# Performance work log

Hardware: AMD Instinct MI355X
Metric: run time of the kernel (lower is better)

Reference implementation:

```python
import jax, jax.numpy as jnp
import numpy as np

N_NODES = 50000
N_PATHS = 4
N_EDGES = 800000
D_IN = 256
D_OUT = 256
D_HID = 128  # SemanticAttention default hidden_size


def setup_inputs() -> dict:
    key = jax.random.key(0)
    ks = jax.random.split(key, 6)
    x = jax.random.normal(ks[0], (N_NODES, D_IN), dtype=jnp.float32)
    edge_indices = jax.random.randint(ks[1], (N_PATHS, 2, N_EDGES), 0, N_NODES)
    Ws = jax.random.normal(ks[2], (N_PATHS, D_IN, D_OUT), dtype=jnp.float32) * (1.0 / np.sqrt(D_IN))
    bs = jnp.zeros((N_PATHS, D_OUT), dtype=jnp.float32)
    attn_w1 = jax.random.normal(ks[3], (D_OUT, D_HID), dtype=jnp.float32) * (1.0 / np.sqrt(D_OUT))
    attn_b1 = jnp.zeros((D_HID,), dtype=jnp.float32)
    attn_w2 = jax.random.normal(ks[4], (D_HID, 1), dtype=jnp.float32) * (1.0 / np.sqrt(D_HID))
    return {"x": x, "edge_indices": edge_indices, "Ws": Ws, "bs": bs,
            "attn_w1": attn_w1, "attn_b1": attn_b1, "attn_w2": attn_w2}


def _gcn_conv(x, W, b, edges):
    """PyG GCNConv with normalize=True, add_self_loops=True.
    out = D^{-1/2} (A + I) D^{-1/2} (x @ W) + b
    """
    n = x.shape[0]
    xw = x @ W  # [N, D_OUT]
    loop = jnp.arange(n, dtype=edges.dtype)
    src = jnp.concatenate([edges[0], loop])
    dst = jnp.concatenate([edges[1], loop])
    ones = jnp.ones(src.shape[0], dtype=x.dtype)
    deg = jax.ops.segment_sum(ones, dst, num_segments=n)  # in-degree incl. self loop
    dinv = jnp.where(deg > 0, jax.lax.rsqrt(deg), 0.0)
    norm = dinv[src] * dinv[dst]  # [E+N]
    msgs = xw[src] * norm[:, None]  # gather + scale
    return jax.ops.segment_sum(msgs, dst, num_segments=n) + b  # scatter-add


def reference(x, edge_indices, Ws, bs, attn_w1, attn_b1, attn_w2):
    P = edge_indices.shape[0]
    # per-meta-path GCN embeddings, stacked -> [N, P, D_OUT]
    z = jnp.stack([_gcn_conv(x, Ws[i], bs[i], edge_indices[i]) for i in range(P)], axis=1)
    # semantic attention: per-node softmax over meta-paths
    w = jnp.tanh(z @ attn_w1 + attn_b1) @ attn_w2  # [N, P, 1]
    beta = jax.nn.softmax(w, axis=1)
    return (beta * z).sum(axis=1)  # [N, D_OUT]
```

## Files before the change

### kernel.cpp

```cpp
#include <hip/hip_runtime.h>
#include <hip/hip_fp16.h>
#include <cstdint>
#include <cstddef>

#define NN 50000
#define NE 800000
#define NP 4
#define DD 256
#define HH 128
#define MPAD 50048
#define PADIDX 50000

#define NB 196
#define CAP 5120
#define SCAP 6144
#define EPB 4096
#define NBB ((NE + EPB - 1) / EPB)
#define BIN_BLOCKS (NBB * NP)

typedef _Float16 f16x8 __attribute__((ext_vector_type(8)));
typedef float f32x4 __attribute__((ext_vector_type(4)));

#define X_OCT (NN * DD / 8)
#define XP_OCT (MPAD * DD / 8)
#define W_OCT (NP * DD * DD / 8)
#define W1_OCT (HH * DD / 8)
#define CVT_BLOCKS ((XP_OCT + W_OCT + W1_OCT + 255) / 256)
#define GEMM_BLOCKS ((MPAD / 64) * NP)

__global__ __launch_bounds__(256) void k_bin(const int* __restrict__ edges,
                                             int* __restrict__ gcnt,
                                             unsigned int* __restrict__ binned,
                                             const float* __restrict__ x,
                                             const float* __restrict__ Ws,
                                             const float* __restrict__ w1,
                                             _Float16* __restrict__ xh,
                                             _Float16* __restrict__ Wt,
                                             _Float16* __restrict__ w1t) {
    const int bx = blockIdx.x;
    const int tid = threadIdx.x;
    if (bx < BIN_BLOCKS) {
        __shared__ int hist[256], lb[256], cur[256], gbase[256], wsum[4];
        __shared__ unsigned int stage[EPB];
        const int p  = bx / NBB;
        const int bc = bx - p * NBB;
        const int e0 = bc * EPB;
        const int total = min(EPB, NE - e0);
        const int* es = edges + (size_t)p * 2 * NE;
        const int* ed = es + NE;
        hist[tid] = 0;
        __syncthreads();
        unsigned int word[16];
        int bkt[16];
#pragma unroll
        for (int j = 0; j < 16; j++) {
            int e = e0 + j * 256 + tid;
            bkt[j] = -1;
            if (e < NE) {
                int dst = ed[e];
                int src = es[e];
                int b = dst >> 8;
                bkt[j] = b;
                word[j] = ((unsigned)b << 24) | ((unsigned)(dst & 255) << 16) | (unsigned)src;
                atomicAdd(&hist[b], 1);
            }
        }
        __syncthreads();
        const int lane = tid & 63, wv = tid >> 6;
        int v = hist[tid];
        int incl = v;
#pragma unroll
        for (int off = 1; off < 64; off <<= 1) {
            int u = __shfl_up(incl, off);
            if (lane >= off) incl += u;
        }
        if (lane == 63) wsum[wv] = incl;
        __syncthreads();
        int wbase = 0;
        for (int i = 0; i < wv; i++) wbase += wsum[i];
        int excl = wbase + incl - v;
        lb[tid] = excl;
        cur[tid] = excl;
        if (tid < NB && v > 0) gbase[tid] = atomicAdd(&gcnt[p * NB + tid], v);
        __syncthreads();
#pragma unroll
        for (int j = 0; j < 16; j++)
            if (bkt[j] >= 0) {
                int r = atomicAdd(&cur[bkt[j]], 1);
                stage[r] = word[j];
            }
        __syncthreads();
        for (int s = tid; s < total; s += 256) {
            unsigned int wd = stage[s];
            int b = wd >> 24;
            int posl = gbase[b] + (s - lb[b]);
            if (posl < CAP)
                binned[(size_t)(p * NB + b) * CAP + posl] = wd & 0x00FFFFFFu;
        }
        return;
    }
    int i = (bx - BIN_BLOCKS) * 256 + tid;
    if (i < XP_OCT) {
        f16x8 o;
        if (i < X_OCT) {
            const float4* src = (const float4*)x + (size_t)i * 2;
            float4 v0 = src[0], v1 = src[1];
            o[0] = (_Float16)v0.x; o[1] = (_Float16)v0.y; o[2] = (_Float16)v0.z; o[3] = (_Float16)v0.w;
            o[4] = (_Float16)v1.x; o[5] = (_Float16)v1.y; o[6] = (_Float16)v1.z; o[7] = (_Float16)v1.w;
        } else {
#pragma unroll
            for (int t = 0; t < 8; t++) o[t] = (_Float16)0.0f;
        }
        *((f16x8*)xh + i) = o;
    } else if (i < XP_OCT + W_OCT) {
        int j = i - XP_OCT;
        int p   = j / (DD * DD / 8);
        int rem = j - p * (DD * DD / 8);
        int n   = rem >> 5;
        int k8  = (rem & 31) * 8;
        const float* wp = Ws + (size_t)p * DD * DD;
        f16x8 o;
#pragma unroll
        for (int t = 0; t < 8; t++) o[t] = (_Float16)wp[(size_t)(k8 + t) * DD + n];
        *((f16x8*)(Wt + (size_t)p * DD * DD + (size_t)n * DD + k8)) = o;
    } else if (i < XP_OCT + W_OCT + W1_OCT) {
        int j = i - XP_OCT - W_OCT;
        int n  = j >> 5;
        int k8 = (j & 31) * 8;
        f16x8 o;
#pragma unroll
        for (int t = 0; t < 8; t++) o[t] = (_Float16)w1[(size_t)(k8 + t) * HH + n];
        *((f16x8*)(w1t + (size_t)n * DD + k8)) = o;
    }
}

__global__ __launch_bounds__(256) void k_sort(const int* __restrict__ gcnt,
                                              const unsigned int* __restrict__ binned,
                                              unsigned short* __restrict__ srcs,
                                              int* __restrict__ offs,
                                              int* __restrict__ ends,
                                              float* __restrict__ dinv) {
    __shared__ int hist[256], cur[256], wsum[4];
    __shared__ unsigned short sorted[SCAP];
    const int bx = blockIdx.x;
    const int tid = threadIdx.x;
    const int p = bx / NB, b = bx - p * NB;
    const int base = bx * SCAP;
    const int n = min(gcnt[bx], CAP);
    hist[tid] = 0;
#pragma unroll
    for (int j = 0; j < SCAP / 256; j++) sorted[j * 256 + tid] = (unsigned short)PADIDX;
    __syncthreads();
    unsigned int w[20];
#pragma unroll
    for (int j = 0; j < 20; j++) {
        int s = j * 256 + tid;
        w[j] = 0xFFFFFFFFu;
        if (s < n) {
            w[j] = binned[(size_t)bx * CAP + s];
            atomicAdd(&hist[(w[j] >> 16) & 255], 1);
        }
    }
    __syncthreads();
    const int lane = tid & 63, wv = tid >> 6;
    int v  = hist[tid];
    int pv = (v + 7) & ~7;
    int incl = pv;
#pragma unroll
    for (int off = 1; off < 64; off <<= 1) {
        int u = __shfl_up(incl, off);
        if (lane >= off) incl += u;
    }
    if (lane == 63) wsum[wv] = incl;
    __syncthreads();
    int wbase = 0;
    for (int i = 0; i < wv; i++) wbase += wsum[i];
    int excl = wbase + incl - pv;
    cur[tid] = excl;
    const int node = b * 256 + tid;
    if (node < NN) {
        int o = base + excl;
        offs[p * NN + node] = o;
        ends[p * NN + node] = o + pv;
        dinv[p * NN + node] = rsqrtf((float)v + 1.0f);
    }
    __syncthreads();
    int totalpad = wsum[0] + wsum[1] + wsum[2] + wsum[3];
#pragma unroll
    for (int j = 0; j < 20; j++)
        if (w[j] != 0xFFFFFFFFu) {
            int r = atomicAdd(&cur[(w[j] >> 16) & 255], 1);
            if (r < SCAP) sorted[r] = (unsigned short)(w[j] & 0xFFFFu);
        }
    __syncthreads();
#pragma unroll
    for (int j = 0; j < SCAP / 256; j++) {
        int s = j * 256 + tid;
        if (s < totalpad && s < SCAP) srcs[base + s] = sorted[s];
    }
}

__global__ __launch_bounds__(256) void k_gemm(const _Float16* __restrict__ xh,
                                              const _Float16* __restrict__ Wt,
                                              const float* __restrict__ dinv,
                                              _Float16* __restrict__ xws) {
    const int gb   = blockIdx.x;
    const int p    = gb / (MPAD / 64);
    const int bm   = gb - p * (MPAD / 64);
    const int wv   = threadIdx.x >> 6;
    const int lane = threadIdx.x & 63;
    const int m_base = bm * 64;
    const int n0   = wv * 64;
    const int mr   = lane & 15;
    const int quad = lane >> 4;

    const _Float16* ap = xh + (size_t)(m_base + mr) * DD + quad * 8;
    const _Float16* bp = Wt + (size_t)p * DD * DD + (size_t)(n0 + mr) * DD + quad * 8;
    const float* dv = dinv + (size_t)p * NN;
    _Float16* cp = xws + (size_t)p * MPAD * DD;

    f32x4 acc[4][4] = {};
    for (int k0 = 0; k0 < DD; k0 += 32) {
        f16x8 a[4], b[4];
#pragma unroll
        for (int i = 0; i < 4; i++) a[i] = *(const f16x8*)(ap + (size_t)i * 16 * DD + k0);
#pragma unroll
        for (int j = 0; j < 4; j++) b[j] = *(const f16x8*)(bp + (size_t)j * 16 * DD + k0);
#pragma unroll
        for (int i = 0; i < 4; i++)
#pragma unroll
            for (int j = 0; j < 4; j++)
                acc[i][j] = __builtin_amdgcn_mfma_f32_16x16x32_f16(a[i], b[j], acc[i][j], 0, 0, 0);
    }
#pragma unroll
    for (int i = 0; i < 4; i++) {
#pragma unroll
        for (int r = 0; r < 4; r++) {
            int row = m_base + i * 16 + quad * 4 + r;
            float d = (row < NN) ? dv[row] : 0.0f;
#pragma unroll
            for (int j = 0; j < 4; j++)
                cp[(size_t)row * DD + n0 + j * 16 + mr] = (_Float16)(d * acc[i][j][r]);
        }
    }
}

__global__ __launch_bounds__(512) void k_fused(const _Float16* __restrict__ xws,
                                               const float* __restrict__ dinv,
                                               const int* __restrict__ offs,
                                               const int* __restrict__ ends,
                                               const unsigned short* __restrict__ srcs,
                                               const float* __restrict__ bs,
                                               const _Float16* __restrict__ w1t,
                                               const float* __restrict__ b1,
                                               const float* __restrict__ w2,
                                               float* __restrict__ out) {
    const int w    = threadIdx.x >> 6;
    const int lane = threadIdx.x & 63;
    const int quad = lane >> 4, mr = lane & 15;
    const int half = lane >> 5, hl = lane & 31;

    __shared__ __align__(16) _Float16 zs[64][264];

    union U { f16x8 v; int i4[4]; };

#pragma unroll 1
    for (int q = 0; q < 2; q++) {
        const int n = blockIdx.x * 16 + w * 2 + q;
#pragma unroll 1
        for (int p = 0; p < NP; p++) {
            const _Float16* xp = xws + (size_t)p * MPAD * DD;
            U acc;
#pragma unroll
            for (int t = 0; t < 4; t++) acc.i4[t] = 0;
            if (half == 0)
                acc.v = *(const f16x8*)(xp + (size_t)n * DD + hl * 8);
            int k  = offs[p * NN + n];
            int ke = ends[p * NN + n];
            for (; k + 16 <= ke; k += 16) {
                int s[8];
#pragma unroll
                for (int j = 0; j < 8; j++) s[j] = srcs[k + 2 * j + half];
                f16x8 v[8];
#pragma unroll
                for (int j = 0; j < 8; j++)
                    v[j] = *(const f16x8*)(xp + (size_t)s[j] * DD + hl * 8);
                acc.v += ((v[0] + v[1]) + (v[2] + v[3])) + ((v[4] + v[5]) + (v[6] + v[7]));
            }
            if (k < ke) {
                int s[4];
#pragma unroll
                for (int j = 0; j < 4; j++) s[j] = srcs[k + 2 * j + half];
                f16x8 v[4];
#pragma unroll
                for (int j = 0; j < 4; j++)
                    v[j] = *(const f16x8*)(xp + (size_t)s[j] * DD + hl * 8);
                acc.v += (v[0] + v[1]) + (v[2] + v[3]);
            }
            U other;
#pragma unroll
            for (int t = 0; t < 4; t++) other.i4[t] = __shfl_xor(acc.i4[t], 32);
            acc.v += other.v;
            if (half == 0) {
                float dvv = dinv[p * NN + n];
                int row = (w * 2 + q) * 4 + p;
                f16x8 zo;
#pragma unroll
                for (int t = 0; t < 8; t++)
                    zo[t] = (_Float16)(dvv * (float)acc.v[t] + bs[p * DD + hl * 8 + t]);
                *(f16x8*)&zs[row][hl * 8] = zo;
            }
        }
    }

    __syncthreads();
    if (w >= 4) return;

    f32x4 acch[8] = {};
    for (int k0 = 0; k0 < DD; k0 += 32) {
        f16x8 a = *(const f16x8*)&zs[w * 16 + mr][k0 + quad * 8];
#pragma unroll
        for (int j = 0; j < 8; j++) {
            f16x8 b = *(const f16x8*)(w1t + (size_t)(j * 16 + mr) * DD + k0 + quad * 8);
            acch[j] = __builtin_amdgcn_mfma_f32_16x16x32_f16(a, b, acch[j], 0, 0, 0);
        }
    }

    float part[4] = {};
#pragma unroll
    for (int j = 0; j < 8; j++) {
        int col = j * 16 + mr;
        float bb = b1[col], ww = w2[col];
#pragma unroll
        for (int r = 0; r < 4; r++)
            part[r] += tanhf(acch[j][r] + bb) * ww;
    }
#pragma unroll
    for (int off = 1; off < 16; off <<= 1) {
#pragma unroll
        for (int r = 0; r < 4; r++) part[r] += __shfl_xor(part[r], off);
    }
    float m = fmaxf(fmaxf(part[0], part[1]), fmaxf(part[2], part[3]));
    float e0 = __expf(part[0] - m), e1 = __expf(part[1] - m),
          e2 = __expf(part[2] - m), e3 = __expf(part[3] - m);
    float rr = 1.0f / (e0 + e1 + e2 + e3);
    float be[4] = {e0 * rr, e1 * rr, e2 * rr, e3 * rr};

    const int n  = blockIdx.x * 16 + w * 4 + quad;
    const int rb = w * 16 + quad * 4;
    float o[16] = {};
#pragma unroll
    for (int p = 0; p < 4; p++) {
        f16x8 z0 = *(const f16x8*)&zs[rb + p][mr * 16];
        f16x8 z1 = *(const f16x8*)&zs[rb + p][mr * 16 + 8];
#pragma unroll
        for (int t = 0; t < 8; t++) {
            o[t]     += be[p] * (float)z0[t];
            o[t + 8] += be[p] * (float)z1[t];
        }
    }
#pragma unroll
    for (int t = 0; t < 16; t += 4)
        *(float4*)(out + (size_t)n * DD + mr * 16 + t) =
            make_float4(o[t], o[t + 1], o[t + 2], o[t + 3]);
}

extern "C" void kernel_launch(void* const* d_in, const int* in_sizes, int n_in,
                              void* d_out, int out_size, void* d_ws, size_t ws_size,
                              hipStream_t stream) {
    const float* x     = (const float*)d_in[0];
    const int*   edges = (const int*)d_in[1];
    const float* Ws    = (const float*)d_in[2];
    const float* bs    = (const float*)d_in[3];
    const float* w1    = (const float*)d_in[4];
    const float* b1    = (const float*)d_in[5];
    const float* w2    = (const float*)d_in[6];
    float* out = (float*)d_out;

    char* ws = (char*)d_ws;
    int*            gcnt   = (int*)ws;
    unsigned int*   binned = (unsigned int*)(ws + (1 << 20));
    unsigned short* srcs   = (unsigned short*)(ws + (18 << 20));
    float*          dinv   = (float*)(ws + (28 << 20));
    int*            offs   = (int*)(ws + (29 << 20));
    int*            ends   = (int*)(ws + (30 << 20));
    _Float16*       Wt     = (_Float16*)(ws + (31 << 20));
    _Float16*       w1t    = (_Float16*)(ws + (31 << 20) + (1 << 19));
    _Float16*       xh     = (_Float16*)(ws + (32 << 20));
    _Float16*       xws    = (_Float16*)(ws + (58 << 20));

    hipMemsetAsync(gcnt, 0, NP * NB * sizeof(int), stream);

    k_bin<<<BIN_BLOCKS + CVT_BLOCKS, 256, 0, stream>>>(
        edges, gcnt, binned, x, Ws, w1, xh, Wt, w1t);

    k_sort<<<NP * NB, 256, 0, stream>>>(gcnt, binned, srcs, offs, ends, dinv);

    k_gemm<<<GEMM_BLOCKS, 256, 0, stream>>>(xh, Wt, dinv, xws);

    k_fused<<<NN / 16, 512, 0, stream>>>(xws, dinv, offs, ends, srcs,
                                         bs, w1t, b1, w2, out);
}
```

Measured before the change: 539.6 us.

## Aggregate raw features before per-path GEMM, fusing GEMM into attention kernel

```diff
diff --git a/kernel.cpp b/kernel.cpp
--- a/kernel.cpp
+++ b/kernel.cpp
@@ -20,13 +20,14 @@
 
 typedef _Float16 f16x8 __attribute__((ext_vector_type(8)));
 typedef float f32x4 __attribute__((ext_vector_type(4)));
+typedef unsigned short u16x8 __attribute__((ext_vector_type(8)));
+typedef unsigned short u16x4 __attribute__((ext_vector_type(4)));
 
 #define X_OCT (NN * DD / 8)
 #define XP_OCT (MPAD * DD / 8)
 #define W_OCT (NP * DD * DD / 8)
 #define W1_OCT (HH * DD / 8)
 #define CVT_BLOCKS ((XP_OCT + W_OCT + W1_OCT + 255) / 256)
-#define GEMM_BLOCKS ((MPAD / 64) * NP)
 
 __global__ __launch_bounds__(256) void k_bin(const int* __restrict__ edges,
                                              int* __restrict__ gcnt,
@@ -182,7 +183,7 @@
         int o = base + excl;
         offs[p * NN + node] = o;
         ends[p * NN + node] = o + pv;
-        dinv[p * NN + node] = rsqrtf((float)v + 1.0f);
+        dinv[(size_t)p * MPAD + node] = rsqrtf((float)v + 1.0f);
     }
     __syncthreads();
     int totalpad = wsum[0] + wsum[1] + wsum[2] + wsum[3];
@@ -200,56 +201,75 @@
     }
 }
 
-__global__ __launch_bounds__(256) void k_gemm(const _Float16* __restrict__ xh,
-                                              const _Float16* __restrict__ Wt,
-                                              const float* __restrict__ dinv,
-                                              _Float16* __restrict__ xws) {
-    const int gb   = blockIdx.x;
-    const int p    = gb / (MPAD / 64);
-    const int bm   = gb - p * (MPAD / 64);
-    const int wv   = threadIdx.x >> 6;
+__global__ __launch_bounds__(256) void k_agg(const _Float16* __restrict__ xh,
+                                             const float* __restrict__ dinv,
+                                             const int* __restrict__ offs,
+                                             const int* __restrict__ ends,
+                                             const unsigned short* __restrict__ srcs,
+                                             _Float16* __restrict__ agg) {
+    const int wv = threadIdx.x >> 6;
     const int lane = threadIdx.x & 63;
-    const int m_base = bm * 64;
-    const int n0   = wv * 64;
-    const int mr   = lane & 15;
-    const int quad = lane >> 4;
-
-    const _Float16* ap = xh + (size_t)(m_base + mr) * DD + quad * 8;
-    const _Float16* bp = Wt + (size_t)p * DD * DD + (size_t)(n0 + mr) * DD + quad * 8;
-    const float* dv = dinv + (size_t)p * NN;
-    _Float16* cp = xws + (size_t)p * MPAD * DD;
-
-    f32x4 acc[4][4] = {};
-    for (int k0 = 0; k0 < DD; k0 += 32) {
-        f16x8 a[4], b[4];
-#pragma unroll
-        for (int i = 0; i < 4; i++) a[i] = *(const f16x8*)(ap + (size_t)i * 16 * DD + k0);
-#pragma unroll
-        for (int j = 0; j < 4; j++) b[j] = *(const f16x8*)(bp + (size_t)j * 16 * DD + k0);
-#pragma unroll
-        for (int i = 0; i < 4; i++)
-#pragma unroll
-            for (int j = 0; j < 4; j++)
-                acc[i][j] = __builtin_amdgcn_mfma_f32_16x16x32_f16(a[i], b[j], acc[i][j], 0, 0, 0);
-    }
-#pragma unroll
-    for (int i = 0; i < 4; i++) {
-#pragma unroll
-        for (int r = 0; r < 4; r++) {
-            int row = m_base + i * 16 + quad * 4 + r;
-            float d = (row < NN) ? dv[row] : 0.0f;
-#pragma unroll
-            for (int j = 0; j < 4; j++)
-                cp[(size_t)row * DD + n0 + j * 16 + mr] = (_Float16)(d * acc[i][j][r]);
-        }
-    }
-}
-
-__global__ __launch_bounds__(512) void k_fused(const _Float16* __restrict__ xws,
-                                               const float* __restrict__ dinv,
-                                               const int* __restrict__ offs,
-                                               const int* __restrict__ ends,
-                                               const unsigned short* __restrict__ srcs,
+    const int half = lane >> 5, hl = lane & 31;
+    const int p = blockIdx.x / (NN / 4);
+    const int n = (blockIdx.x - p * (NN / 4)) * 4 + wv;
+    const float* dvp = dinv + (size_t)p * MPAD;
+
+    const float dd = dvp[n];
+    float facc[8];
+    {
+        f16x8 xv = *(const f16x8*)(xh + (size_t)n * DD + hl * 8);
+#pragma unroll
+        for (int t = 0; t < 8; t++) facc[t] = (half == 0) ? dd * (float)xv[t] : 0.0f;
+    }
+
+    int k  = offs[p * NN + n];
+    int ke = ends[p * NN + n];
+    for (; k + 16 <= ke; k += 16) {
+        u16x8 su = *(const u16x8*)(srcs + k + half * 8);
+        int s[8];
+#pragma unroll
+        for (int j = 0; j < 8; j++) s[j] = su[j];
+        f16x8 v[8];
+#pragma unroll
+        for (int j = 0; j < 8; j++)
+            v[j] = *(const f16x8*)(xh + (size_t)s[j] * DD + hl * 8);
+        float dv[8];
+#pragma unroll
+        for (int j = 0; j < 8; j++) dv[j] = dvp[s[j]];
+#pragma unroll
+        for (int j = 0; j < 8; j++)
+#pragma unroll
+            for (int t = 0; t < 8; t++) facc[t] += dv[j] * (float)v[j][t];
+    }
+    if (k < ke) {
+        u16x4 su = *(const u16x4*)(srcs + k + half * 4);
+        int s[4];
+#pragma unroll
+        for (int j = 0; j < 4; j++) s[j] = su[j];
+        f16x8 v[4];
+#pragma unroll
+        for (int j = 0; j < 4; j++)
+            v[j] = *(const f16x8*)(xh + (size_t)s[j] * DD + hl * 8);
+        float dv[4];
+#pragma unroll
+        for (int j = 0; j < 4; j++) dv[j] = dvp[s[j]];
+#pragma unroll
+        for (int j = 0; j < 4; j++)
+#pragma unroll
+            for (int t = 0; t < 8; t++) facc[t] += dv[j] * (float)v[j][t];
+    }
+#pragma unroll
+    for (int t = 0; t < 8; t++) facc[t] += __shfl_xor(facc[t], 32);
+    if (half == 0) {
+        f16x8 o;
+#pragma unroll
+        for (int t = 0; t < 8; t++) o[t] = (_Float16)(dd * facc[t]);
+        *(f16x8*)(agg + ((size_t)p * NN + n) * DD + hl * 8) = o;
+    }
+}
+
+__global__ __launch_bounds__(512) void k_zattn(const _Float16* __restrict__ agg,
+                                               const _Float16* __restrict__ Wt,
                                                const float* __restrict__ bs,
                                                const _Float16* __restrict__ w1t,
                                                const float* __restrict__ b1,
@@ -258,58 +278,32 @@
     const int w    = threadIdx.x >> 6;
     const int lane = threadIdx.x & 63;
     const int quad = lane >> 4, mr = lane & 15;
-    const int half = lane >> 5, hl = lane & 31;
 
     __shared__ __align__(16) _Float16 zs[64][264];
 
-    union U { f16x8 v; int i4[4]; };
-
-#pragma unroll 1
-    for (int q = 0; q < 2; q++) {
-        const int n = blockIdx.x * 16 + w * 2 + q;
-#pragma unroll 1
-        for (int p = 0; p < NP; p++) {
-            const _Float16* xp = xws + (size_t)p * MPAD * DD;
-            U acc;
-#pragma unroll
-            for (int t = 0; t < 4; t++) acc.i4[t] = 0;
-            if (half == 0)
-                acc.v = *(const f16x8*)(xp + (size_t)n * DD + hl * 8);
-            int k  = offs[p * NN + n];
-            int ke = ends[p * NN + n];
-            for (; k + 16 <= ke; k += 16) {
-                int s[8];
-#pragma unroll
-                for (int j = 0; j < 8; j++) s[j] = srcs[k + 2 * j + half];
-                f16x8 v[8];
-#pragma unroll
-                for (int j = 0; j < 8; j++)
-                    v[j] = *(const f16x8*)(xp + (size_t)s[j] * DD + hl * 8);
-                acc.v += ((v[0] + v[1]) + (v[2] + v[3])) + ((v[4] + v[5]) + (v[6] + v[7]));
+    const int n0 = blockIdx.x * 16;
+
+    {
+        const int p  = w & 3;
+        const int nh = w >> 2;
+        const _Float16* ap = agg + ((size_t)p * NN + n0 + mr) * DD + quad * 8;
+        const _Float16* bp = Wt + (size_t)p * DD * DD + (size_t)(nh * 128 + mr) * DD + quad * 8;
+        f32x4 acc[8] = {};
+        for (int k0 = 0; k0 < DD; k0 += 32) {
+            f16x8 a = *(const f16x8*)(ap + k0);
+#pragma unroll
+            for (int j = 0; j < 8; j++) {
+                f16x8 b = *(const f16x8*)(bp + (size_t)(j * 16) * DD + k0);
+                acc[j] = __builtin_amdgcn_mfma_f32_16x16x32_f16(a, b, acc[j], 0, 0, 0);
             }
-            if (k < ke) {
-                int s[4];
-#pragma unroll
-                for (int j = 0; j < 4; j++) s[j] = srcs[k + 2 * j + half];
-                f16x8 v[4];
-#pragma unroll
-                for (int j = 0; j < 4; j++)
-                    v[j] = *(const f16x8*)(xp + (size_t)s[j] * DD + hl * 8);
-                acc.v += (v[0] + v[1]) + (v[2] + v[3]);
-            }
-            U other;
-#pragma unroll
-            for (int t = 0; t < 4; t++) other.i4[t] = __shfl_xor(acc.i4[t], 32);
-            acc.v += other.v;
-            if (half == 0) {
-                float dvv = dinv[p * NN + n];
-                int row = (w * 2 + q) * 4 + p;
-                f16x8 zo;
-#pragma unroll
-                for (int t = 0; t < 8; t++)
-                    zo[t] = (_Float16)(dvv * (float)acc.v[t] + bs[p * DD + hl * 8 + t]);
-                *(f16x8*)&zs[row][hl * 8] = zo;
-            }
+        }
+#pragma unroll
+        for (int j = 0; j < 8; j++) {
+            int col = nh * 128 + j * 16 + mr;
+            float bb = bs[p * DD + col];
+#pragma unroll
+            for (int r = 0; r < 4; r++)
+                zs[(quad * 4 + r) * 4 + p][col] = (_Float16)(acc[j][r] + bb);
         }
     }
 
@@ -387,17 +381,17 @@
     _Float16*       Wt     = (_Float16*)(ws + (31 << 20));
     _Float16*       w1t    = (_Float16*)(ws + (31 << 20) + (1 << 19));
     _Float16*       xh     = (_Float16*)(ws + (32 << 20));
-    _Float16*       xws    = (_Float16*)(ws + (58 << 20));
+    _Float16*       agg    = (_Float16*)(ws + (58 << 20));
 
     hipMemsetAsync(gcnt, 0, NP * NB * sizeof(int), stream);
+    hipMemsetAsync(dinv, 0, (size_t)NP * MPAD * sizeof(float), stream);
 
     k_bin<<<BIN_BLOCKS + CVT_BLOCKS, 256, 0, stream>>>(
         edges, gcnt, binned, x, Ws, w1, xh, Wt, w1t);
 
     k_sort<<<NP * NB, 256, 0, stream>>>(gcnt, binned, srcs, offs, ends, dinv);
 
-    k_gemm<<<GEMM_BLOCKS, 256, 0, stream>>>(xh, Wt, dinv, xws);
-
-    k_fused<<<NN / 16, 512, 0, stream>>>(xws, dinv, offs, ends, srcs,
-                                         bs, w1t, b1, w2, out);
-}
+    k_agg<<<NP * NN / 4, 256, 0, stream>>>(xh, dinv, offs, ends, srcs, agg);
+
+    k_zattn<<<NN / 16, 512, 0, stream>>>(agg, Wt, bs, w1t, b1, w2, out);
+}
```

Result: slower. 683.5 us (+26.7%).
